# Kernel tuning notes

Hardware: AMD Instinct MI355X
Metric: run time of the kernel (lower is better)

The kernel has to match this reference:

```python
import jax, jax.numpy as jnp
import numpy as np

IN_FEATURES = 3
CODE_NUM = 64
CODE_CHANNEL = 64
SHAPE_NUM = 1


def setup_inputs() -> dict:
    key = jax.random.key(0)
    k1, k2 = jax.random.split(key)
    coords = jax.random.uniform(k1, (8, 65536, IN_FEATURES), dtype=jnp.float32)  # in [0,1) subset of [-1,1]
    table_size = SHAPE_NUM * CODE_NUM ** IN_FEATURES
    # xavier_uniform for [C, N] matrix
    limit = float(np.sqrt(6.0 / (CODE_CHANNEL + table_size)))
    shape_code = jax.random.uniform(k2, (CODE_CHANNEL, table_size), dtype=jnp.float32,
                                    minval=-limit, maxval=limit)
    return {"coords": coords, "shape_code": shape_code, "idx": 0}


def reference(coords, shape_code, idx):
    D = IN_FEATURES
    # corner offset mask: [2^D, D] of {0,1}
    mask = jnp.stack(jnp.meshgrid(*([jnp.arange(2, dtype=jnp.float32)] * D), indexing="ij"), -1)
    mask = mask.reshape(-1, D)                                   # [8, 3]
    mul = jnp.asarray([CODE_NUM ** i for i in range(D)], dtype=jnp.int64)
    offset = jnp.asarray(idx, dtype=jnp.int64) * (CODE_NUM ** D)

    c = (coords + 1.0) * ((CODE_NUM - 1) / 2.0)                  # [B, P, 3] in [0, code_num-1]
    corners = jnp.floor(c)[..., None, :] + mask                  # [B, P, 8, 3]
    coordsf = c[..., None, :] - corners                          # [B, P, 8, 3]
    index = jnp.sum(corners.astype(jnp.int64) * mul, axis=-1) + offset  # [B, P, 8]
    weights = jnp.prod(1.0 - jnp.abs(coordsf), axis=-1)          # [B, P, 8]

    code = jnp.take(shape_code, index, axis=1)                   # [C, B, P, 8] gather
    out = jnp.einsum("cbpk,bpk->bpc", code, weights)             # weighted corner sum
    return out
```

## Files before the change

kernel.cpp:

```cpp
#include <hip/hip_runtime.h>


#define CODE_NUM 64
#define CODE_CHANNEL 64
#define TABLE (CODE_NUM * CODE_NUM * CODE_NUM)

__global__ __launch_bounds__(256) void transpose_k(const float* __restrict__ src,
                                                   float* __restrict__ dst) {
    __shared__ float tile[64 * 65];
    const int t0 = blockIdx.x * 64;
    const int j = threadIdx.x;

#pragma unroll
    for (int i = 0; i < 4; ++i) {
        const int q = (i << 8) | j;
        const int c = q >> 4;
        const int tc4 = q & 15;
        const float4 v = *(const float4*)(src + (size_t)c * TABLE + t0 + (tc4 << 2));
        tile[((tc4 << 2) + 0) * 65 + c] = v.x;
        tile[((tc4 << 2) + 1) * 65 + c] = v.y;
        tile[((tc4 << 2) + 2) * 65 + c] = v.z;
        tile[((tc4 << 2) + 3) * 65 + c] = v.w;
    }
    __syncthreads();

#pragma unroll
    for (int i = 0; i < 4; ++i) {
        const int q = (i << 8) | j;
        const int t = q >> 4;
        const int c4 = q & 15;
        float4 v;
        v.x = tile[t * 65 + (c4 << 2) + 0];
        v.y = tile[t * 65 + (c4 << 2) + 1];
        v.z = tile[t * 65 + (c4 << 2) + 2];
        v.w = tile[t * 65 + (c4 << 2) + 3];
        *(float4*)(dst + (size_t)(t0 + t) * 64 + (c4 << 2)) = v;
    }
}

__global__ __launch_bounds__(256) void interp4_k(const float* __restrict__ coords,
                                                 const float* __restrict__ table,
                                                 const int* __restrict__ idxp,
                                                 float* __restrict__ out,
                                                 int npoints) {
    const unsigned tid = blockIdx.x * 256u + threadIdx.x;
    const int lane = threadIdx.x & 63;
    const int sub = lane >> 4;
    const int cg = lane & 15;
    const int p = (int)((tid >> 6) * 4u + (unsigned)sub);
    if (p >= npoints) return;

    const int offset = idxp[0] * TABLE;

    const float sx = (coords[p * 3 + 0] + 1.0f) * ((CODE_NUM - 1) * 0.5f);
    const float sy = (coords[p * 3 + 1] + 1.0f) * ((CODE_NUM - 1) * 0.5f);
    const float sz = (coords[p * 3 + 2] + 1.0f) * ((CODE_NUM - 1) * 0.5f);

    const float fx = floorf(sx), fy = floorf(sy), fz = floorf(sz);
    const float rx = sx - fx, ry = sy - fy, rz = sz - fz;
    const int ix = (int)fx, iy = (int)fy, iz = (int)fz;
    const int base = offset + ix + iy * CODE_NUM + iz * (CODE_NUM * CODE_NUM);

    const float wx[2] = {1.0f - rx, rx};
    const float wy[2] = {1.0f - ry, ry};
    const float wz[2] = {1.0f - rz, rz};

    const char* tp = (const char*)table;
    const int cgoff = cg << 4;

    float4 acc = make_float4(0.f, 0.f, 0.f, 0.f);
#pragma unroll
    for (int k = 0; k < 8; ++k) {
        const int a = k & 1, b = (k >> 1) & 1, c = (k >> 2) & 1;
        const int idx = base + a + b * CODE_NUM + c * (CODE_NUM * CODE_NUM);
        const float w = wx[a] * wy[b] * wz[c];
        const float4 v = *(const float4*)(tp + ((size_t)(unsigned)(idx << 8) + cgoff));
        acc.x = fmaf(w, v.x, acc.x);
        acc.y = fmaf(w, v.y, acc.y);
        acc.z = fmaf(w, v.z, acc.z);
        acc.w = fmaf(w, v.w, acc.w);
    }
    *(float4*)(out + (size_t)p * CODE_CHANNEL + (cg << 2)) = acc;
}

__global__ __launch_bounds__(256) void interp_fallback_k(const float* __restrict__ coords,
                                                         const float* __restrict__ table,
                                                         const int* __restrict__ idxp,
                                                         float* __restrict__ out,
                                                         int npoints) {
    const int p = (int)((blockIdx.x * 256u + threadIdx.x) >> 6);
    const int lane = threadIdx.x & 63;
    if (p >= npoints) return;
    const int offset = idxp[0] * TABLE;
    const float sx = (coords[p * 3 + 0] + 1.0f) * ((CODE_NUM - 1) * 0.5f);
    const float sy = (coords[p * 3 + 1] + 1.0f) * ((CODE_NUM - 1) * 0.5f);
    const float sz = (coords[p * 3 + 2] + 1.0f) * ((CODE_NUM - 1) * 0.5f);
    const float fx = floorf(sx), fy = floorf(sy), fz = floorf(sz);
    const float rx = sx - fx, ry = sy - fy, rz = sz - fz;
    const int base = offset + (int)fx + (int)fy * CODE_NUM + (int)fz * (CODE_NUM * CODE_NUM);
    const float wx[2] = {1.0f - rx, rx};
    const float wy[2] = {1.0f - ry, ry};
    const float wz[2] = {1.0f - rz, rz};
    float acc = 0.0f;
#pragma unroll
    for (int k = 0; k < 8; ++k) {
        const int a = k & 1, b = (k >> 1) & 1, c = (k >> 2) & 1;
        const int idx = base + a + b * CODE_NUM + c * (CODE_NUM * CODE_NUM);
        acc = fmaf(wx[a] * wy[b] * wz[c], table[(size_t)lane * TABLE + idx], acc);
    }
    out[(size_t)p * CODE_CHANNEL + lane] = acc;
}

extern "C" void kernel_launch(void* const* d_in, const int* in_sizes, int n_in,
                              void* d_out, int out_size, void* d_ws, size_t ws_size,
                              hipStream_t stream) {
    const float* coords = (const float*)d_in[0];
    const float* code   = (const float*)d_in[1];
    const int*   idxp   = (const int*)d_in[2];
    float* out = (float*)d_out;

    const int npoints = in_sizes[0] / 3;
    const size_t tbytes = (size_t)TABLE * CODE_CHANNEL * sizeof(float);

    if (ws_size >= tbytes) {
        float* tt = (float*)d_ws;
        transpose_k<<<TABLE / 64, 256, 0, stream>>>(code, tt);
        interp4_k<<<(npoints + 15) / 16, 256, 0, stream>>>(coords, tt, idxp, out, npoints);
    } else {
        interp_fallback_k<<<(npoints + 3) / 4, 256, 0, stream>>>(coords, code, idxp, out, npoints);
    }
}
```

Measured before the change: 280.8 us.

## Bin-sort points by cell and transpose only the touched table region

Adds a pass that histograms the points into 4x4x4-cell bins. A scan and a scatter then reorder the points so the interpolation kernel visits spatially nearby points together, which should raise cache reuse of the gathered corner rows. A bounding box on the y/z cell indices is computed in the same pass, and the transposition of the code table skips slabs no point can touch. The interpolation grid is also block-swizzled, and results are written back through the stored original index. In exchange it adds several small launches, atomics on a global cursor and an extra sorted-coordinate buffer in workspace.

```diff
diff --git a/kernel.cpp b/kernel.cpp
--- a/kernel.cpp
+++ b/kernel.cpp
@@ -4,13 +4,107 @@
 #define CODE_NUM 64
 #define CODE_CHANNEL 64
 #define TABLE (CODE_NUM * CODE_NUM * CODE_NUM)
-
-__global__ __launch_bounds__(256) void transpose_k(const float* __restrict__ src,
-                                                   float* __restrict__ dst) {
+#define NBINS 4096
+
+__global__ __launch_bounds__(256) void init_k(int* __restrict__ hist, int* __restrict__ bbox) {
+    const int t = blockIdx.x * 256 + threadIdx.x;
+    for (int i = t; i < NBINS; i += gridDim.x * 256) hist[i] = 0;
+    if (t == 0) {
+        bbox[0] = 0x7fffffff; bbox[1] = (int)0x80000000;
+        bbox[2] = 0x7fffffff; bbox[3] = (int)0x80000000;
+    }
+}
+
+__device__ __forceinline__ int cell_bin(float x, float y, float z,
+                                        int& ix, int& iy, int& iz) {
+    ix = (int)floorf((x + 1.0f) * ((CODE_NUM - 1) * 0.5f));
+    iy = (int)floorf((y + 1.0f) * ((CODE_NUM - 1) * 0.5f));
+    iz = (int)floorf((z + 1.0f) * ((CODE_NUM - 1) * 0.5f));
+    const int cx = min(max(ix, 0), 63) >> 2;
+    const int cy = min(max(iy, 0), 63) >> 2;
+    const int cz = min(max(iz, 0), 63) >> 2;
+    return cx | (cy << 4) | (cz << 8);
+}
+
+__global__ __launch_bounds__(256) void hist_bbox_k(const float* __restrict__ coords, int npoints,
+                                                   int* __restrict__ hist, int* __restrict__ bbox) {
+    __shared__ int lh[NBINS];
+    __shared__ int lb[4];
+    for (int i = threadIdx.x; i < NBINS; i += 256) lh[i] = 0;
+    if (threadIdx.x == 0) {
+        lb[0] = 0x7fffffff; lb[1] = (int)0x80000000;
+        lb[2] = 0x7fffffff; lb[3] = (int)0x80000000;
+    }
+    __syncthreads();
+    int ymin = 0x7fffffff, ymax = (int)0x80000000;
+    int zmin = 0x7fffffff, zmax = (int)0x80000000;
+    const int stride = gridDim.x * 256;
+    for (int p = blockIdx.x * 256 + threadIdx.x; p < npoints; p += stride) {
+        const float x = coords[p * 3 + 0];
+        const float y = coords[p * 3 + 1];
+        const float z = coords[p * 3 + 2];
+        int ix, iy, iz;
+        const int bin = cell_bin(x, y, z, ix, iy, iz);
+        atomicAdd(&lh[bin], 1);
+        ymin = min(ymin, iy); ymax = max(ymax, iy);
+        zmin = min(zmin, iz); zmax = max(zmax, iz);
+    }
+    atomicMin(&lb[0], ymin); atomicMax(&lb[1], ymax);
+    atomicMin(&lb[2], zmin); atomicMax(&lb[3], zmax);
+    __syncthreads();
+    for (int i = threadIdx.x; i < NBINS; i += 256) {
+        const int c = lh[i];
+        if (c) atomicAdd(&hist[i], c);
+    }
+    if (threadIdx.x == 0) {
+        atomicMin(&bbox[0], lb[0]); atomicMax(&bbox[1], lb[1]);
+        atomicMin(&bbox[2], lb[2]); atomicMax(&bbox[3], lb[3]);
+    }
+}
+
+__global__ __launch_bounds__(64) void scan_k(const int* __restrict__ hist, int* __restrict__ cursor) {
+    const int l = threadIdx.x;
+    int s = 0;
+#pragma unroll 1
+    for (int i = 0; i < 64; ++i) s += hist[l * 64 + i];
+    int inc = s;
+#pragma unroll
+    for (int d = 1; d < 64; d <<= 1) {
+        const int u = __shfl_up(inc, d, 64);
+        if (l >= d) inc += u;
+    }
+    int run = inc - s;
+#pragma unroll 1
+    for (int i = 0; i < 64; ++i) {
+        cursor[l * 64 + i] = run;
+        run += hist[l * 64 + i];
+    }
+}
+
+__global__ __launch_bounds__(256) void scatter_k(const float* __restrict__ coords, int npoints,
+                                                 int* __restrict__ cursor, float4* __restrict__ sorted) {
+    const int stride = gridDim.x * 256;
+    for (int p = blockIdx.x * 256 + threadIdx.x; p < npoints; p += stride) {
+        const float x = coords[p * 3 + 0];
+        const float y = coords[p * 3 + 1];
+        const float z = coords[p * 3 + 2];
+        int ix, iy, iz;
+        const int bin = cell_bin(x, y, z, ix, iy, iz);
+        const int slot = atomicAdd(&cursor[bin], 1);
+        sorted[slot] = make_float4(x, y, z, __int_as_float(p));
+    }
+}
+
+__global__ __launch_bounds__(256) void transpose_bb_k(const float* __restrict__ src,
+                                                      float* __restrict__ dst,
+                                                      const int* __restrict__ bbox) {
+    const int t0 = blockIdx.x * 64;
+    const int y = (t0 >> 6) & 63;
+    const int z = t0 >> 12;
+    if (y < bbox[0] || y > bbox[1] + 1 || z < bbox[2] || z > bbox[3] + 1) return;
+
     __shared__ float tile[64 * 65];
-    const int t0 = blockIdx.x * 64;
     const int j = threadIdx.x;
-
 #pragma unroll
     for (int i = 0; i < 4; ++i) {
         const int q = (i << 8) | j;
@@ -23,7 +117,6 @@
         tile[((tc4 << 2) + 3) * 65 + c] = v.w;
     }
     __syncthreads();
-
 #pragma unroll
     for (int i = 0; i < 4; ++i) {
         const int q = (i << 8) | j;
@@ -36,6 +129,88 @@
         v.w = tile[t * 65 + (c4 << 2) + 3];
         *(float4*)(dst + (size_t)(t0 + t) * 64 + (c4 << 2)) = v;
     }
+}
+
+__global__ __launch_bounds__(256) void transpose_k(const float* __restrict__ src,
+                                                   float* __restrict__ dst) {
+    __shared__ float tile[64 * 65];
+    const int t0 = blockIdx.x * 64;
+    const int j = threadIdx.x;
+#pragma unroll
+    for (int i = 0; i < 4; ++i) {
+        const int q = (i << 8) | j;
+        const int c = q >> 4;
+        const int tc4 = q & 15;
+        const float4 v = *(const float4*)(src + (size_t)c * TABLE + t0 + (tc4 << 2));
+        tile[((tc4 << 2) + 0) * 65 + c] = v.x;
+        tile[((tc4 << 2) + 1) * 65 + c] = v.y;
+        tile[((tc4 << 2) + 2) * 65 + c] = v.z;
+        tile[((tc4 << 2) + 3) * 65 + c] = v.w;
+    }
+    __syncthreads();
+#pragma unroll
+    for (int i = 0; i < 4; ++i) {
+        const int q = (i << 8) | j;
+        const int t = q >> 4;
+        const int c4 = q & 15;
+        float4 v;
+        v.x = tile[t * 65 + (c4 << 2) + 0];
+        v.y = tile[t * 65 + (c4 << 2) + 1];
+        v.z = tile[t * 65 + (c4 << 2) + 2];
+        v.w = tile[t * 65 + (c4 << 2) + 3];
+        *(float4*)(dst + (size_t)(t0 + t) * 64 + (c4 << 2)) = v;
+    }
+}
+
+__global__ __launch_bounds__(256) void interp4s_k(const float4* __restrict__ sorted,
+                                                  const float* __restrict__ table,
+                                                  const int* __restrict__ idxp,
+                                                  float* __restrict__ out,
+                                                  int npoints) {
+    unsigned bid = blockIdx.x;
+    const unsigned nb = gridDim.x;
+    if ((nb & 7u) == 0u) {
+        const unsigned c = nb >> 3;
+        bid = (bid & 7u) * c + (bid >> 3);
+    }
+    const int lane = threadIdx.x & 63;
+    const int sub = lane >> 4;
+    const int cg = lane & 15;
+    const int p = (int)(bid * 16u + ((threadIdx.x >> 6) << 2) + (unsigned)sub);
+    if (p >= npoints) return;
+
+    const int offset = idxp[0] * TABLE;
+    const float4 s4 = sorted[p];
+    const int op = __float_as_int(s4.w);
+
+    const float sx = (s4.x + 1.0f) * ((CODE_NUM - 1) * 0.5f);
+    const float sy = (s4.y + 1.0f) * ((CODE_NUM - 1) * 0.5f);
+    const float sz = (s4.z + 1.0f) * ((CODE_NUM - 1) * 0.5f);
+    const float fx = floorf(sx), fy = floorf(sy), fz = floorf(sz);
+    const float rx = sx - fx, ry = sy - fy, rz = sz - fz;
+    const int ix = (int)fx, iy = (int)fy, iz = (int)fz;
+    const int base = offset + ix + iy * CODE_NUM + iz * (CODE_NUM * CODE_NUM);
+
+    const float wx[2] = {1.0f - rx, rx};
+    const float wy[2] = {1.0f - ry, ry};
+    const float wz[2] = {1.0f - rz, rz};
+
+    const char* tp = (const char*)table;
+    const int cgoff = cg << 4;
+
+    float4 acc = make_float4(0.f, 0.f, 0.f, 0.f);
+#pragma unroll
+    for (int k = 0; k < 8; ++k) {
+        const int a = k & 1, b = (k >> 1) & 1, c = (k >> 2) & 1;
+        const int idx = base + a + b * CODE_NUM + c * (CODE_NUM * CODE_NUM);
+        const float w = wx[a] * wy[b] * wz[c];
+        const float4 v = *(const float4*)(tp + ((size_t)(unsigned)(idx << 8) + cgoff));
+        acc.x = fmaf(w, v.x, acc.x);
+        acc.y = fmaf(w, v.y, acc.y);
+        acc.z = fmaf(w, v.z, acc.z);
+        acc.w = fmaf(w, v.w, acc.w);
+    }
+    *(float4*)(out + (size_t)op * CODE_CHANNEL + (cg << 2)) = acc;
 }
 
 __global__ __launch_bounds__(256) void interp4_k(const float* __restrict__ coords,
@@ -51,23 +226,18 @@
     if (p >= npoints) return;
 
     const int offset = idxp[0] * TABLE;
-
     const float sx = (coords[p * 3 + 0] + 1.0f) * ((CODE_NUM - 1) * 0.5f);
     const float sy = (coords[p * 3 + 1] + 1.0f) * ((CODE_NUM - 1) * 0.5f);
     const float sz = (coords[p * 3 + 2] + 1.0f) * ((CODE_NUM - 1) * 0.5f);
-
     const float fx = floorf(sx), fy = floorf(sy), fz = floorf(sz);
     const float rx = sx - fx, ry = sy - fy, rz = sz - fz;
     const int ix = (int)fx, iy = (int)fy, iz = (int)fz;
     const int base = offset + ix + iy * CODE_NUM + iz * (CODE_NUM * CODE_NUM);
-
     const float wx[2] = {1.0f - rx, rx};
     const float wy[2] = {1.0f - ry, ry};
     const float wz[2] = {1.0f - rz, rz};
-
     const char* tp = (const char*)table;
     const int cgoff = cg << 4;
-
     float4 acc = make_float4(0.f, 0.f, 0.f, 0.f);
 #pragma unroll
     for (int k = 0; k < 8; ++k) {
@@ -121,8 +291,24 @@
 
     const int npoints = in_sizes[0] / 3;
     const size_t tbytes = (size_t)TABLE * CODE_CHANNEL * sizeof(float);
-
-    if (ws_size >= tbytes) {
+    const size_t sbytes = (size_t)npoints * sizeof(float4);
+    const size_t need = tbytes + sbytes + 2 * NBINS * sizeof(int) + 64;
+
+    if (ws_size >= need) {
+        char* w = (char*)d_ws;
+        float*  tt     = (float*)w;
+        float4* sorted = (float4*)(w + tbytes);
+        int*    hist   = (int*)(w + tbytes + sbytes);
+        int*    cursor = hist + NBINS;
+        int*    bbox   = cursor + NBINS;
+
+        init_k<<<16, 256, 0, stream>>>(hist, bbox);
+        hist_bbox_k<<<256, 256, 0, stream>>>(coords, npoints, hist, bbox);
+        scan_k<<<1, 64, 0, stream>>>(hist, cursor);
+        transpose_bb_k<<<TABLE / 64, 256, 0, stream>>>(code, tt, bbox);
+        scatter_k<<<256, 256, 0, stream>>>(coords, npoints, cursor, sorted);
+        interp4s_k<<<(npoints + 15) / 16, 256, 0, stream>>>(sorted, tt, idxp, out, npoints);
+    } else if (ws_size >= tbytes) {
         float* tt = (float*)d_ws;
         transpose_k<<<TABLE / 64, 256, 0, stream>>>(code, tt);
         interp4_k<<<(npoints + 15) / 16, 256, 0, stream>>>(coords, tt, idxp, out, npoints);
```

Result: slower. 364.7 us (+29.9%).
